# Kernel optimization log

Measured on AMD Instinct MI355X. Metric: run time of the kernel, lower is better.

The kernel has to match this reference:

```python
import jax, jax.numpy as jnp
import numpy as np

B, N, D_FEAT = 16, 4096, 64
NPOINT, NSAMPLE = 1024, 32
MLP = [64, 64, 128]
IN_CH = 3 + D_FEAT
EPS = 1e-5  # BatchNorm eps (torch default)


def _fps(xyz, npoint):
    # Farthest point sampling; sequential scan over npoint steps (matches torch loop).
    b, n, _ = xyz.shape
    def step(carry, _):
        distance, farthest = carry  # (B,N) running min dist, (B,) current centroid idx
        centroid = jnp.take_along_axis(xyz, farthest[:, None, None], axis=1)  # (B,1,3)
        d = jnp.sum((xyz - centroid) ** 2, -1)  # (B,N)
        distance = jnp.minimum(distance, d)
        nxt = jnp.argmax(distance, -1).astype(jnp.int32)
        return (distance, nxt), farthest
    init = (jnp.full((b, n), jnp.inf, dtype=xyz.dtype),
            jnp.full((b,), n // 2, dtype=jnp.int32))
    _, centroids = jax.lax.scan(step, init, None, length=npoint)
    return centroids.T  # (B, npoint)


def _gather(pts, idx):
    # pts: (B,N,C); idx: (B,...) int -> (B,...,C)
    return jax.vmap(lambda p, i: p[i])(pts, idx)


def setup_inputs() -> dict:
    key = jax.random.key(0)
    ks = jax.random.split(key, 16)
    inp = {
        'xyz': jax.random.normal(ks[0], (B, N, 3), jnp.float32),
        'points': jax.random.normal(ks[1], (B, N, D_FEAT), jnp.float32),
    }
    last = IN_CH
    for li, oc in enumerate(MLP):
        inp[f'W{li}'] = jax.random.normal(ks[2 + li], (oc, last), jnp.float32) * (1.0 / np.sqrt(last))
        inp[f'b{li}'] = jnp.zeros((oc,), jnp.float32)
        inp[f'g{li}'] = jnp.ones((oc,), jnp.float32)
        inp[f'be{li}'] = jnp.zeros((oc,), jnp.float32)
        last = oc
    C = MLP[-1]; R = C // 8
    inp['aW1'] = jax.random.normal(ks[10], (R, C), jnp.float32) * (1.0 / np.sqrt(C))
    inp['aW2'] = jax.random.normal(ks[11], (C, R), jnp.float32) * (1.0 / np.sqrt(R))
    return inp


def reference(xyz, points, W0, b0, g0, be0, W1, b1, g1, be1, W2, b2, g2, be2, aW1, aW2):
    fps_idx = _fps(xyz, NPOINT)                 # (B,S) int32
    new_xyz = _gather(xyz, fps_idx)             # (B,S,3)
    # squared distances (B,S,N) via matmul expansion (as torch square_distance)
    d = (-2.0 * jnp.einsum('bsc,bnc->bsn', new_xyz, xyz)
         + jnp.sum(new_xyz ** 2, -1)[..., None]
         + jnp.sum(xyz ** 2, -1)[:, None, :])
    _, idx = jax.lax.top_k(-d, NSAMPLE)         # (B,S,k) nearest neighbors
    grouped_xyz = _gather(xyz, idx)             # (B,S,k,3)
    rel = grouped_xyz - new_xyz[:, :, None, :]  # relative coords
    feat = _gather(points, idx)                 # (B,S,k,D)
    g = jnp.concatenate([rel, feat], axis=-1)   # (B,S,k,3+D) channels-last
    # 1x1 conv MLP + BatchNorm (training-mode batch stats) + ReLU
    for (W, b, ga, be) in ((W0, b0, g0, be0), (W1, b1, g1, be1), (W2, b2, g2, be2)):
        g = jnp.einsum('bskc,oc->bsko', g, W) + b
        mu = g.mean(axis=(0, 1, 2))
        var = g.var(axis=(0, 1, 2))
        g = ga * (g - mu) * jax.lax.rsqrt(var + EPS) + be
        g = jax.nn.relu(g)
    new_points = g.max(axis=2)                  # max over nsample -> (B,S,C)
    # channel attention on (B,C,S) == reductions over S here
    avg = new_points.mean(axis=1)               # (B,C)
    mx = new_points.max(axis=1)                 # (B,C)
    def fc(v):
        return jnp.einsum('cr,br->bc', aW2, jax.nn.relu(jnp.einsum('rc,bc->br', aW1, v)))
    scale = jax.nn.sigmoid(fc(avg) + fc(mx))    # (B,C)
    new_points = new_points * scale[:, None, :]
    return new_xyz, new_points, fps_idx
```

## Files before the change

kernel.cpp:

```cpp
#include <hip/hip_runtime.h>
#include <hip/hip_bf16.h>

#define BB 16
#define NN 4096
#define SS 1024
#define KS 32
#define DF 64
#define INC 67
#define C1 64
#define C2 64
#define C3 128
#define ROWS (BB*SS*KS)
#define EPSBN 1e-5f
#define F_INF (__builtin_inff())

typedef __bf16 bf16;
typedef __bf16 bfrag __attribute__((ext_vector_type(8)));
typedef float  ffrag __attribute__((ext_vector_type(4)));
typedef unsigned long long u64;

#define OUT_NXYZ 0
#define OUT_NP   49152
#define OUT_FPS  2146304

#define OFF_FPS   0u
#define OFF_NXYZ  65536u
#define OFF_IDX   262144u
#define OFF_STATS 2359296u
#define OFF_ASUM  2555904u
#define OFF_AMAX  2621440u
#define OFF_BNC   2686976u
#define OFF_SCALE 2690048u
#define OFF_NP0   2698240u
#define OFF_YMAX  11086848u
#define OFF_H1    19475456u
#define OFF_H2    86584320u
#define ZERO_BYTES (196608u + 65536u + 65536u)

__device__ __forceinline__ u64 dpp_max16(u64 key){
  {
    int lo = __builtin_amdgcn_update_dpp((int)(unsigned)key, (int)(unsigned)key, 0xB1, 0xf, 0xf, true);
    int hi = __builtin_amdgcn_update_dpp((int)(key>>32), (int)(key>>32), 0xB1, 0xf, 0xf, true);
    u64 k2 = ((u64)(unsigned)hi<<32)|(unsigned)lo;
    key = k2 > key ? k2 : key;
  }
  {
    int lo = __builtin_amdgcn_update_dpp((int)(unsigned)key, (int)(unsigned)key, 0x4E, 0xf, 0xf, true);
    int hi = __builtin_amdgcn_update_dpp((int)(key>>32), (int)(key>>32), 0x4E, 0xf, 0xf, true);
    u64 k2 = ((u64)(unsigned)hi<<32)|(unsigned)lo;
    key = k2 > key ? k2 : key;
  }
  {
    int lo = __builtin_amdgcn_update_dpp((int)(unsigned)key, (int)(unsigned)key, 0x141, 0xf, 0xf, true);
    int hi = __builtin_amdgcn_update_dpp((int)(key>>32), (int)(key>>32), 0x141, 0xf, 0xf, true);
    u64 k2 = ((u64)(unsigned)hi<<32)|(unsigned)lo;
    key = k2 > key ? k2 : key;
  }
  {
    int lo = __builtin_amdgcn_update_dpp((int)(unsigned)key, (int)(unsigned)key, 0x140, 0xf, 0xf, true);
    int hi = __builtin_amdgcn_update_dpp((int)(key>>32), (int)(key>>32), 0x140, 0xf, 0xf, true);
    u64 k2 = ((u64)(unsigned)hi<<32)|(unsigned)lo;
    key = k2 > key ? k2 : key;
  }
  return key;
}

__global__ __launch_bounds__(256) void fps_kernel(const float* __restrict__ xyz,
                                                  int* __restrict__ fps_i,
                                                  float* __restrict__ nxyz_ws,
                                                  float* __restrict__ out)
{
  __shared__ float lx[NN], ly[NN], lz[NN];
  __shared__ int lfps[SS];
  __shared__ u64 slotk[2][16];
  int b = blockIdx.x, t = threadIdx.x;
  const float* xb = xyz + (size_t)b*NN*3;
  for (int p = t; p < NN; p += 256){ lx[p]=xb[p*3]; ly[p]=xb[p*3+1]; lz[p]=xb[p*3+2]; }
  __syncthreads();
  float px[16],py[16],pz[16],pd[16];
  int p0 = t*16;
  #pragma unroll
  for (int j=0;j<16;++j){ px[j]=lx[p0+j]; py[j]=ly[p0+j]; pz[j]=lz[p0+j]; pd[j]=F_INF; }
  float cx = lx[NN/2], cy = ly[NN/2], cz = lz[NN/2];
  if (t==0) lfps[0]=NN/2;
  for (int it=1; it<SS; ++it){
    float bv=-1.f; int bi=p0;
    #pragma unroll
    for (int j=0;j<16;++j){
      float dx=px[j]-cx, dy=py[j]-cy, dz=pz[j]-cz;
      float d = __fadd_rn(__fadd_rn(__fmul_rn(dx,dx),__fmul_rn(dy,dy)),__fmul_rn(dz,dz));
      float nd = fminf(pd[j], d);
      pd[j]=nd;
      if (nd > bv){ bv=nd; bi=p0+j; }
    }
    u64 key = ((u64)__float_as_uint(bv) << 32) | (unsigned)(~bi);
    key = dpp_max16(key);
    int p = it & 1;
    if ((t & 15) == 0) slotk[p][t>>4] = key;
    __syncthreads();
    u64 k = slotk[p][t & 15];
    k = dpp_max16(k);
    int i = ~(unsigned)k;
    cx = lx[i]; cy = ly[i]; cz = lz[i];
    if (t==0) lfps[it]=i;
  }
  __syncthreads();
  for (int s=t; s<SS; s+=256){
    int i = lfps[s];
    fps_i[b*SS+s]=i;
    out[OUT_FPS + b*SS + s] = (float)i;
    float xx=lx[i], yy=ly[i], zz=lz[i];
    int o3 = (b*SS+s)*3;
    out[OUT_NXYZ+o3]=xx; out[OUT_NXYZ+o3+1]=yy; out[OUT_NXYZ+o3+2]=zz;
    nxyz_ws[o3]=xx; nxyz_ws[o3+1]=yy; nxyz_ws[o3+2]=zz;
  }
}

__global__ __launch_bounds__(64) void knn_kernel(const float* __restrict__ xyz,
                                                 const float* __restrict__ nxyz,
                                                 int* __restrict__ knn)
{
  __shared__ float ld[NN];
  int lane = threadIdx.x;
  int bs = blockIdx.x;
  int b = bs >> 10;
  const float* xb = xyz + (size_t)b*NN*3;
  float sx=nxyz[bs*3], sy=nxyz[bs*3+1], sz=nxyz[bs*3+2];
  float gv[8]; int gi[8];
  float lv = F_INF; int li = 0;
  #pragma unroll
  for (int g=0; g<8; ++g){
    float bgv = F_INF; int bgi = 0;
    #pragma unroll
    for (int jj=0; jj<8; ++jj){
      int p = (g*8+jj)*64 + lane;
      float dx=xb[p*3]-sx, dy=xb[p*3+1]-sy, dz=xb[p*3+2]-sz;
      float d = dx*dx+dy*dy+dz*dz;
      ld[p] = d;
      if (d < bgv){ bgv=d; bgi=p; }
    }
    gv[g]=bgv; gi[g]=bgi;
    if (bgv < lv){ lv=bgv; li=bgi; }
  }
  int kept = 0;
  for (int it=0; it<KS; ++it){
    float v=lv; int i=li;
    #pragma unroll
    for (int o=32;o;o>>=1){
      float v2=__shfl_xor(v,o); int i2=__shfl_xor(i,o);
      if (v2<v || (v2==v && i2<i)){ v=v2; i=i2; }
    }
    if (lane==it) kept = i;
    if ((i & 63) == lane){
      int j = i >> 6;
      ld[i] = F_INF;
      int g = j >> 3;
      float bgv=F_INF; int bgi=0;
      for (int jj=0;jj<8;++jj){
        int p = (g*8+jj)*64 + lane;
        float d = ld[p];
        if (d<bgv){bgv=d;bgi=p;}
      }
      #pragma unroll
      for (int q=0;q<8;++q){ if (q==g){ gv[q]=bgv; gi[q]=bgi; } }
      lv=F_INF; li=0;
      #pragma unroll
      for (int q=0;q<8;++q){ if (gv[q]<lv){ lv=gv[q]; li=gi[q]; } }
    }
  }
  if (lane < KS) knn[bs*KS + lane] = kept;
}

__global__ __launch_bounds__(256) void conv1_kernel(const float* __restrict__ xyz,
                                                    const float* __restrict__ points,
                                                    const float* __restrict__ W0,
                                                    const float* __restrict__ b0,
                                                    const float* __restrict__ nxyz,
                                                    const int* __restrict__ knn,
                                                    bf16* __restrict__ h1,
                                                    float* __restrict__ stats)
{
  __shared__ __align__(16) bf16 As[64][104];
  __shared__ __align__(16) bf16 Bs[64][104];
  __shared__ float s1[C1], s2[C1];
  int t = threadIdx.x;
  int Rbase = blockIdx.x * 64;
  if (t < C1){ s1[t]=0.f; s2[t]=0.f; }
  {
    int o = t >> 2, q = t & 3;
    const float* wr = W0 + o*INC;
    for (int cc = q*24; cc < q*24+24; ++cc){
      float w;
      if (cc < 64) w = wr[3+cc];
      else if (cc < 67) w = wr[cc-64];
      else w = 0.f;
      Bs[o][cc] = (bf16)w;
    }
  }
  {
    int r = t >> 2, q = t & 3;
    int R = Rbase + r;
    int bs = R >> 5;
    int bIdx = bs >> 10;
    int nI = knn[R];
    const float* pr = points + ((size_t)(bIdx*NN + nI))*DF + q*16;
    float4 f0 = *(const float4*)(pr);
    float4 f1 = *(const float4*)(pr+4);
    float4 f2 = *(const float4*)(pr+8);
    float4 f3 = *(const float4*)(pr+12);
    bf16* ap = &As[r][q*16];
    ap[0]=(bf16)f0.x; ap[1]=(bf16)f0.y; ap[2]=(bf16)f0.z; ap[3]=(bf16)f0.w;
    ap[4]=(bf16)f1.x; ap[5]=(bf16)f1.y; ap[6]=(bf16)f1.z; ap[7]=(bf16)f1.w;
    ap[8]=(bf16)f2.x; ap[9]=(bf16)f2.y; ap[10]=(bf16)f2.z; ap[11]=(bf16)f2.w;
    ap[12]=(bf16)f3.x; ap[13]=(bf16)f3.y; ap[14]=(bf16)f3.z; ap[15]=(bf16)f3.w;
    if (q==0){
      const float* xr = xyz + ((size_t)(bIdx*NN + nI))*3;
      const float* nr = nxyz + bs*3;
      As[r][64]=(bf16)(xr[0]-nr[0]);
      As[r][65]=(bf16)(xr[1]-nr[1]);
      As[r][66]=(bf16)(xr[2]-nr[2]);
      for (int cc=67; cc<96; ++cc) As[r][cc]=(bf16)0.f;
    }
  }
  __syncthreads();
  int wv = t >> 6, lane = t & 63;
  int row16 = wv * 16;
  int arow = lane & 15, kgrp = lane >> 4;
  ffrag acc[4] = {};
  #pragma unroll
  for (int kc = 0; kc < 3; ++kc){
    bfrag af = *(const bfrag*)&As[row16 + arow][kc*32 + kgrp*8];
    #pragma unroll
    for (int nt = 0; nt < 4; ++nt){
      bfrag bfv = *(const bfrag*)&Bs[nt*16 + arow][kc*32 + kgrp*8];
      acc[nt] = __builtin_amdgcn_mfma_f32_16x16x32_bf16(af, bfv, acc[nt], 0,0,0);
    }
  }
  #pragma unroll
  for (int nt=0; nt<4; ++nt){
    int c = nt*16 + arow;
    float bias = b0[c];
    float ls1=0.f, ls2=0.f;
    #pragma unroll
    for (int r=0;r<4;++r){
      float y = acc[nt][r] + bias;
      int grow = Rbase + row16 + kgrp*4 + r;
      h1[(size_t)grow*C1 + c] = (bf16)y;
      ls1 += y; ls2 += y*y;
    }
    ls1 += __shfl_xor(ls1, 16); ls1 += __shfl_xor(ls1, 32);
    ls2 += __shfl_xor(ls2, 16); ls2 += __shfl_xor(ls2, 32);
    if (kgrp==0){ atomicAdd(&s1[c], ls1); atomicAdd(&s2[c], ls2); }
  }
  __syncthreads();
  if (t < C1){
    float* gp = stats + (blockIdx.x & 63)*256;
    atomicAdd(&gp[t], s1[t]);
    atomicAdd(&gp[128 + t], s2[t]);
  }
}

__global__ void bnfin_kernel(const float* __restrict__ stats, const float* __restrict__ g,
                             const float* __restrict__ be, float* __restrict__ bnc, int C)
{
  int c = threadIdx.x; if (c >= C) return;
  float a1=0.f, a2=0.f;
  for (int q=0;q<64;++q){ a1 += stats[q*256+c]; a2 += stats[q*256+128+c]; }
  float inv = 1.f/(float)ROWS;
  float mu = a1*inv; float var = a2*inv - mu*mu;
  float a = g[c]*rsqrtf(var + EPSBN);
  bnc[c] = a; bnc[128+c] = be[c] - mu*a;
}

__global__ __launch_bounds__(256) void conv2_kernel(const bf16* __restrict__ h1,
                                                    const float* __restrict__ W1,
                                                    const float* __restrict__ b1,
                                                    const float* __restrict__ bnc,
                                                    bf16* __restrict__ h2,
                                                    float* __restrict__ stats)
{
  __shared__ __align__(16) bf16 As[64][72];
  __shared__ __align__(16) bf16 Bs[64][72];
  __shared__ float s1[C2], s2[C2];
  int t = threadIdx.x;
  int Rbase = blockIdx.x * 64;
  if (t < C2){ s1[t]=0.f; s2[t]=0.f; }
  {
    int o = t >> 2, q = t & 3;
    const float* wr = W1 + o*64 + q*16;
    bf16* bp = &Bs[o][q*16];
    #pragma unroll
    for (int v=0; v<4; ++v){
      float4 f = *(const float4*)(wr + v*4);
      bp[v*4+0]=(bf16)f.x; bp[v*4+1]=(bf16)f.y; bp[v*4+2]=(bf16)f.z; bp[v*4+3]=(bf16)f.w;
    }
  }
  {
    int r = t >> 2, q = t & 3;
    int R = Rbase + r;
    const bf16* hr = h1 + (size_t)R*64 + q*16;
    bfrag h0 = *(const bfrag*)hr;
    bfrag h1v = *(const bfrag*)(hr+8);
    #pragma unroll
    for (int j=0;j<8;++j){
      int c=q*16+j;
      As[r][c] = (bf16)fmaxf(fmaf(bnc[c], (float)h0[j], bnc[128+c]), 0.f);
    }
    #pragma unroll
    for (int j=0;j<8;++j){
      int c=q*16+8+j;
      As[r][c] = (bf16)fmaxf(fmaf(bnc[c], (float)h1v[j], bnc[128+c]), 0.f);
    }
  }
  __syncthreads();
  int wv = t >> 6, lane = t & 63;
  int row16 = wv * 16;
  int arow = lane & 15, kgrp = lane >> 4;
  ffrag acc[4] = {};
  #pragma unroll
  for (int kc = 0; kc < 2; ++kc){
    bfrag af = *(const bfrag*)&As[row16 + arow][kc*32 + kgrp*8];
    #pragma unroll
    for (int nt = 0; nt < 4; ++nt){
      bfrag bfv = *(const bfrag*)&Bs[nt*16 + arow][kc*32 + kgrp*8];
      acc[nt] = __builtin_amdgcn_mfma_f32_16x16x32_bf16(af, bfv, acc[nt], 0,0,0);
    }
  }
  #pragma unroll
  for (int nt=0; nt<4; ++nt){
    int c = nt*16 + arow;
    float bias = b1[c];
    float ls1=0.f, ls2=0.f;
    #pragma unroll
    for (int r=0;r<4;++r){
      float y = acc[nt][r] + bias;
      int grow = Rbase + row16 + kgrp*4 + r;
      h2[(size_t)grow*C2 + c] = (bf16)y;
      ls1 += y; ls2 += y*y;
    }
    ls1 += __shfl_xor(ls1, 16); ls1 += __shfl_xor(ls1, 32);
    ls2 += __shfl_xor(ls2, 16); ls2 += __shfl_xor(ls2, 32);
    if (kgrp==0){ atomicAdd(&s1[c], ls1); atomicAdd(&s2[c], ls2); }
  }
  __syncthreads();
  if (t < C2){
    float* gp = stats + (blockIdx.x & 63)*256;
    atomicAdd(&gp[t], s1[t]);
    atomicAdd(&gp[128 + t], s2[t]);
  }
}

__global__ __launch_bounds__(256) void conv3_kernel(const bf16* __restrict__ h2,
                                                    const float* __restrict__ W2,
                                                    const float* __restrict__ b2,
                                                    const float* __restrict__ bnc,
                                                    float* __restrict__ ymax,
                                                    float* __restrict__ stats)
{
  __shared__ __align__(16) bf16 As[64][72];
  __shared__ __align__(16) bf16 Bs[128][72];
  __shared__ float s1[C3], s2[C3];
  __shared__ float wmax[4][C3];
  int t = threadIdx.x;
  int Rbase = blockIdx.x * 64;
  if (t < C3){ s1[t]=0.f; s2[t]=0.f; }
  {
    int o = t >> 1, q = t & 1;
    const float* wr = W2 + o*64 + q*32;
    bf16* bp = &Bs[o][q*32];
    #pragma unroll
    for (int v=0; v<8; ++v){
      float4 f = *(const float4*)(wr + v*4);
      bp[v*4+0]=(bf16)f.x; bp[v*4+1]=(bf16)f.y; bp[v*4+2]=(bf16)f.z; bp[v*4+3]=(bf16)f.w;
    }
  }
  {
    int r = t >> 2, q = t & 3;
    int R = Rbase + r;
    const bf16* hr = h2 + (size_t)R*64 + q*16;
    bfrag h0 = *(const bfrag*)hr;
    bfrag h1v = *(const bfrag*)(hr+8);
    #pragma unroll
    for (int j=0;j<8;++j){
      int c=q*16+j;
      As[r][c] = (bf16)fmaxf(fmaf(bnc[c], (float)h0[j], bnc[128+c]), 0.f);
    }
    #pragma unroll
    for (int j=0;j<8;++j){
      int c=q*16+8+j;
      As[r][c] = (bf16)fmaxf(fmaf(bnc[c], (float)h1v[j], bnc[128+c]), 0.f);
    }
  }
  __syncthreads();
  int wv = t >> 6, lane = t & 63;
  int row16 = wv * 16;
  int arow = lane & 15, kgrp = lane >> 4;
  ffrag acc[8] = {};
  #pragma unroll
  for (int kc = 0; kc < 2; ++kc){
    bfrag af = *(const bfrag*)&As[row16 + arow][kc*32 + kgrp*8];
    #pragma unroll
    for (int nt = 0; nt < 8; ++nt){
      bfrag bfv = *(const bfrag*)&Bs[nt*16 + arow][kc*32 + kgrp*8];
      acc[nt] = __builtin_amdgcn_mfma_f32_16x16x32_bf16(af, bfv, acc[nt], 0,0,0);
    }
  }
  #pragma unroll
  for (int nt=0; nt<8; ++nt){
    int c = nt*16 + arow;
    float bias = b2[c];
    float ls1=0.f, ls2=0.f, mm=-F_INF;
    #pragma unroll
    for (int r=0;r<4;++r){
      float y = acc[nt][r] + bias;
      ls1 += y; ls2 += y*y; mm = fmaxf(mm, y);
    }
    ls1 += __shfl_xor(ls1, 16); ls1 += __shfl_xor(ls1, 32);
    ls2 += __shfl_xor(ls2, 16); ls2 += __shfl_xor(ls2, 32);
    mm = fmaxf(mm, __shfl_xor(mm, 16)); mm = fmaxf(mm, __shfl_xor(mm, 32));
    if (kgrp==0){ atomicAdd(&s1[c], ls1); atomicAdd(&s2[c], ls2); wmax[wv][c]=mm; }
  }
  __syncthreads();
  {
    int half = t >> 7;
    int c = t & 127;
    float m = fmaxf(wmax[half*2][c], wmax[half*2+1][c]);
    ymax[(size_t)(blockIdx.x*2 + half)*C3 + c] = m;
  }
  if (t < C3){
    float* gp = stats + (blockIdx.x & 63)*256;
    atomicAdd(&gp[t], s1[t]);
    atomicAdd(&gp[128 + t], s2[t]);
  }
}

__global__ __launch_bounds__(256) void attreduce_kernel(const float* __restrict__ ymax,
                                                        const float* __restrict__ bnc,
                                                        float* __restrict__ np0,
                                                        float* __restrict__ asum,
                                                        unsigned* __restrict__ amax)
{
  __shared__ float rs[256], rm[256];
  int t = threadIdx.x;
  int b = blockIdx.x >> 3, sg = blockIdx.x & 7;
  int c = t & 127, h = t >> 7;
  float a = bnc[c], bb = bnc[128+c];
  size_t base = ((size_t)(b*1024 + sg*128 + h*64))*128 + c;
  float s = 0.f, m = 0.f;
  #pragma unroll 4
  for (int j=0;j<64;++j){
    float v = fmaxf(fmaf(a, ymax[base + (size_t)j*128], bb), 0.f);
    np0[base + (size_t)j*128] = v;
    s += v; m = fmaxf(m, v);
  }
  rs[t]=s; rm[t]=m;
  __syncthreads();
  if (t < 128){
    float s2 = rs[t] + rs[t+128];
    float m2 = fmaxf(rm[t], rm[t+128]);
    atomicAdd(&asum[b*128+t], s2);
    atomicMax(&amax[b*128+t], __float_as_uint(m2));
  }
}

__global__ __launch_bounds__(256) void attn_kernel(const float* __restrict__ asum,
                                                   const unsigned* __restrict__ amax,
                                                   const float* __restrict__ aW1,
                                                   const float* __restrict__ aW2,
                                                   float* __restrict__ scale)
{
  __shared__ float avg[16][128], mx[16][128], hA[16][16], hM[16][16];
  int t = threadIdx.x;
  for (int i=t; i<2048; i+=256){
    int b=i>>7, c=i&127;
    avg[b][c]=asum[i]*(1.f/1024.f); mx[b][c]=__uint_as_float(amax[i]);
  }
  __syncthreads();
  {
    int b=t>>4, r=t&15;
    float sa=0.f, sm=0.f;
    for (int c=0;c<128;++c){ float w=aW1[r*128+c]; sa+=w*avg[b][c]; sm+=w*mx[b][c]; }
    hA[b][r]=fmaxf(sa,0.f); hM[b][r]=fmaxf(sm,0.f);
  }
  __syncthreads();
  for (int i=t;i<2048;i+=256){
    int b=i>>7,c=i&127;
    float o=0.f;
    for (int r=0;r<16;++r){ o += aW2[c*16+r]*(hA[b][r]+hM[b][r]); }
    scale[i] = 1.f/(1.f+expf(-o));
  }
}

__global__ __launch_bounds__(256) void finout_kernel(const float* __restrict__ np0,
                                                     const float* __restrict__ scale,
                                                     float* __restrict__ out)
{
  int i = blockIdx.x*256 + threadIdx.x;
  int c = i & 127; int b = i >> 17;
  out[OUT_NP + i] = np0[i] * scale[b*128+c];
}

extern "C" void kernel_launch(void* const* d_in, const int* in_sizes, int n_in,
                              void* d_out, int out_size, void* d_ws, size_t ws_size,
                              hipStream_t stream)
{
  const float* xyz    = (const float*)d_in[0];
  const float* points = (const float*)d_in[1];
  const float* W0 = (const float*)d_in[2];
  const float* b0 = (const float*)d_in[3];
  const float* g0 = (const float*)d_in[4];
  const float* be0= (const float*)d_in[5];
  const float* W1 = (const float*)d_in[6];
  const float* b1 = (const float*)d_in[7];
  const float* g1 = (const float*)d_in[8];
  const float* be1= (const float*)d_in[9];
  const float* W2 = (const float*)d_in[10];
  const float* b2 = (const float*)d_in[11];
  const float* g2 = (const float*)d_in[12];
  const float* be2= (const float*)d_in[13];
  const float* aW1= (const float*)d_in[14];
  const float* aW2= (const float*)d_in[15];
  float* out = (float*)d_out;
  char* ws = (char*)d_ws;

  int*      fpsI  = (int*)(ws + OFF_FPS);
  float*    nxyz  = (float*)(ws + OFF_NXYZ);
  int*      knnI  = (int*)(ws + OFF_IDX);
  float*    stats = (float*)(ws + OFF_STATS);
  float*    asum  = (float*)(ws + OFF_ASUM);
  unsigned* amax  = (unsigned*)(ws + OFF_AMAX);
  float*    bnc   = (float*)(ws + OFF_BNC);
  float*    scl   = (float*)(ws + OFF_SCALE);
  float*    np0   = (float*)(ws + OFF_NP0);
  float*    ymax  = (float*)(ws + OFF_YMAX);
  bf16*     h1    = (bf16*)(ws + OFF_H1);
  bf16*     h2    = (bf16*)(ws + OFF_H2);

  hipMemsetAsync(ws + OFF_STATS, 0, ZERO_BYTES, stream);
  fps_kernel<<<BB, 256, 0, stream>>>(xyz, fpsI, nxyz, out);
  knn_kernel<<<BB*SS, 64, 0, stream>>>(xyz, nxyz, knnI);
  conv1_kernel<<<ROWS/64, 256, 0, stream>>>(xyz, points, W0, b0, nxyz, knnI, h1, stats);
  bnfin_kernel<<<1, 128, 0, stream>>>(stats, g0, be0, bnc, C1);
  conv2_kernel<<<ROWS/64, 256, 0, stream>>>(h1, W1, b1, bnc, h2, stats + 64*256);
  bnfin_kernel<<<1, 128, 0, stream>>>(stats + 64*256, g1, be1, bnc + 256, C2);
  conv3_kernel<<<ROWS/64, 256, 0, stream>>>(h2, W2, b2, bnc + 256, ymax, stats + 2*64*256);
  bnfin_kernel<<<1, 128, 0, stream>>>(stats + 2*64*256, g2, be2, bnc + 512, C3);
  attreduce_kernel<<<BB*8, 256, 0, stream>>>(ymax, bnc + 512, np0, asum, amax);
  attn_kernel<<<1, 256, 0, stream>>>(asum, amax, aW1, aW2, scl);
  finout_kernel<<<(BB*SS*C3)/256, 256, 0, stream>>>(np0, scl, out);
}
```

Baseline: 1.202 ms.

## Use full-wave DPP reductions and packed float2 math in FPS and kNN

Replaces the 16-lane DPP argmax with a full 64-lane DPP reduction (row_shr plus row_bcast) followed by a lane-63 broadcast. This cuts the cross-wave slot exchange in FPS from 16 to 4 entries and replaces the shuffle-based argmin in the kNN selection loop. Point coordinates are stored as float4 in LDS so the centroid lookup is a single load, and distance math uses float2 vectors to allow packed FP32 instructions. FP contraction is disabled so the distance rounding stays the same; the risk is that the bcast DPP semantics or the lane-63 broadcast pick the wrong winner.

```diff
diff --git a/kernel.cpp b/kernel.cpp
--- a/kernel.cpp
+++ b/kernel.cpp
@@ -17,6 +17,7 @@
 typedef __bf16 bf16;
 typedef __bf16 bfrag __attribute__((ext_vector_type(8)));
 typedef float  ffrag __attribute__((ext_vector_type(4)));
+typedef float  f2    __attribute__((ext_vector_type(2)));
 typedef unsigned long long u64;
 
 #define OUT_NXYZ 0
@@ -37,32 +38,20 @@
 #define OFF_H2    86584320u
 #define ZERO_BYTES (196608u + 65536u + 65536u)
 
-__device__ __forceinline__ u64 dpp_max16(u64 key){
-  {
-    int lo = __builtin_amdgcn_update_dpp((int)(unsigned)key, (int)(unsigned)key, 0xB1, 0xf, 0xf, true);
-    int hi = __builtin_amdgcn_update_dpp((int)(key>>32), (int)(key>>32), 0xB1, 0xf, 0xf, true);
-    u64 k2 = ((u64)(unsigned)hi<<32)|(unsigned)lo;
-    key = k2 > key ? k2 : key;
-  }
-  {
-    int lo = __builtin_amdgcn_update_dpp((int)(unsigned)key, (int)(unsigned)key, 0x4E, 0xf, 0xf, true);
-    int hi = __builtin_amdgcn_update_dpp((int)(key>>32), (int)(key>>32), 0x4E, 0xf, 0xf, true);
-    u64 k2 = ((u64)(unsigned)hi<<32)|(unsigned)lo;
-    key = k2 > key ? k2 : key;
-  }
-  {
-    int lo = __builtin_amdgcn_update_dpp((int)(unsigned)key, (int)(unsigned)key, 0x141, 0xf, 0xf, true);
-    int hi = __builtin_amdgcn_update_dpp((int)(key>>32), (int)(key>>32), 0x141, 0xf, 0xf, true);
-    u64 k2 = ((u64)(unsigned)hi<<32)|(unsigned)lo;
-    key = k2 > key ? k2 : key;
-  }
-  {
-    int lo = __builtin_amdgcn_update_dpp((int)(unsigned)key, (int)(unsigned)key, 0x140, 0xf, 0xf, true);
-    int hi = __builtin_amdgcn_update_dpp((int)(key>>32), (int)(key>>32), 0x140, 0xf, 0xf, true);
-    u64 k2 = ((u64)(unsigned)hi<<32)|(unsigned)lo;
-    key = k2 > key ? k2 : key;
-  }
-  return key;
+#define DPP_MAX_STEP(k, ctrl, rmask, bc) { \
+  int _lo = __builtin_amdgcn_update_dpp(0, (int)(unsigned)(k), (ctrl), (rmask), 0xf, (bc)); \
+  int _hi = __builtin_amdgcn_update_dpp(0, (int)((k)>>32),     (ctrl), (rmask), 0xf, (bc)); \
+  u64 _k2 = ((u64)(unsigned)_hi << 32) | (unsigned)_lo; \
+  if (_k2 > (k)) (k) = _k2; }
+
+__device__ __forceinline__ u64 dpp_wavemax64(u64 k){
+  DPP_MAX_STEP(k, 0x111, 0xf, true)
+  DPP_MAX_STEP(k, 0x112, 0xf, true)
+  DPP_MAX_STEP(k, 0x114, 0xf, true)
+  DPP_MAX_STEP(k, 0x118, 0xf, true)
+  DPP_MAX_STEP(k, 0x142, 0xa, false)
+  DPP_MAX_STEP(k, 0x143, 0xc, false)
+  return k;
 }
 
 __global__ __launch_bounds__(256) void fps_kernel(const float* __restrict__ xyz,
@@ -70,38 +59,51 @@
                                                   float* __restrict__ nxyz_ws,
                                                   float* __restrict__ out)
 {
-  __shared__ float lx[NN], ly[NN], lz[NN];
+  #pragma clang fp contract(off)
+  __shared__ __align__(16) float4 lc[NN];
   __shared__ int lfps[SS];
-  __shared__ u64 slotk[2][16];
+  __shared__ u64 slotk[2][4];
   int b = blockIdx.x, t = threadIdx.x;
   const float* xb = xyz + (size_t)b*NN*3;
-  for (int p = t; p < NN; p += 256){ lx[p]=xb[p*3]; ly[p]=xb[p*3+1]; lz[p]=xb[p*3+2]; }
-  __syncthreads();
-  float px[16],py[16],pz[16],pd[16];
+  for (int p = t; p < NN; p += 256){
+    lc[p] = make_float4(xb[p*3], xb[p*3+1], xb[p*3+2], 0.f);
+  }
+  __syncthreads();
+  f2 px2[8], py2[8], pz2[8], pd2[8];
   int p0 = t*16;
   #pragma unroll
-  for (int j=0;j<16;++j){ px[j]=lx[p0+j]; py[j]=ly[p0+j]; pz[j]=lz[p0+j]; pd[j]=F_INF; }
-  float cx = lx[NN/2], cy = ly[NN/2], cz = lz[NN/2];
+  for (int j=0;j<8;++j){
+    float4 a = lc[p0+2*j], c = lc[p0+2*j+1];
+    px2[j] = (f2){a.x, c.x}; py2[j] = (f2){a.y, c.y}; pz2[j] = (f2){a.z, c.z};
+    pd2[j] = (f2){F_INF, F_INF};
+  }
+  float cx = lc[NN/2].x, cy = lc[NN/2].y, cz = lc[NN/2].z;
   if (t==0) lfps[0]=NN/2;
+  int wv = t >> 6, lane = t & 63;
   for (int it=1; it<SS; ++it){
+    f2 c2x = (f2){cx,cx}, c2y = (f2){cy,cy}, c2z = (f2){cz,cz};
     float bv=-1.f; int bi=p0;
     #pragma unroll
-    for (int j=0;j<16;++j){
-      float dx=px[j]-cx, dy=py[j]-cy, dz=pz[j]-cz;
-      float d = __fadd_rn(__fadd_rn(__fmul_rn(dx,dx),__fmul_rn(dy,dy)),__fmul_rn(dz,dz));
-      float nd = fminf(pd[j], d);
-      pd[j]=nd;
-      if (nd > bv){ bv=nd; bi=p0+j; }
+    for (int j=0;j<8;++j){
+      f2 dx = px2[j]-c2x, dy = py2[j]-c2y, dz = pz2[j]-c2z;
+      f2 d = (dx*dx + dy*dy) + dz*dz;
+      f2 nd = (f2){fminf(pd2[j].x, d.x), fminf(pd2[j].y, d.y)};
+      pd2[j]=nd;
+      if (nd.x > bv){ bv=nd.x; bi=p0+2*j; }
+      if (nd.y > bv){ bv=nd.y; bi=p0+2*j+1; }
     }
     u64 key = ((u64)__float_as_uint(bv) << 32) | (unsigned)(~bi);
-    key = dpp_max16(key);
+    key = dpp_wavemax64(key);
+    key = __shfl(key, 63);
     int p = it & 1;
-    if ((t & 15) == 0) slotk[p][t>>4] = key;
+    if (lane == 0) slotk[p][wv] = key;
     __syncthreads();
-    u64 k = slotk[p][t & 15];
-    k = dpp_max16(k);
+    u64 k = slotk[p][t & 3];
+    DPP_MAX_STEP(k, 0xB1, 0xf, true)
+    DPP_MAX_STEP(k, 0x4E, 0xf, true)
     int i = ~(unsigned)k;
-    cx = lx[i]; cy = ly[i]; cz = lz[i];
+    float4 cc = lc[i];
+    cx = cc.x; cy = cc.y; cz = cc.z;
     if (t==0) lfps[it]=i;
   }
   __syncthreads();
@@ -109,10 +111,10 @@
     int i = lfps[s];
     fps_i[b*SS+s]=i;
     out[OUT_FPS + b*SS + s] = (float)i;
-    float xx=lx[i], yy=ly[i], zz=lz[i];
+    float4 cc = lc[i];
     int o3 = (b*SS+s)*3;
-    out[OUT_NXYZ+o3]=xx; out[OUT_NXYZ+o3+1]=yy; out[OUT_NXYZ+o3+2]=zz;
-    nxyz_ws[o3]=xx; nxyz_ws[o3+1]=yy; nxyz_ws[o3+2]=zz;
+    out[OUT_NXYZ+o3]=cc.x; out[OUT_NXYZ+o3+1]=cc.y; out[OUT_NXYZ+o3+2]=cc.z;
+    nxyz_ws[o3]=cc.x; nxyz_ws[o3+1]=cc.y; nxyz_ws[o3+2]=cc.z;
   }
 }
 
@@ -144,12 +146,10 @@
   }
   int kept = 0;
   for (int it=0; it<KS; ++it){
-    float v=lv; int i=li;
-    #pragma unroll
-    for (int o=32;o;o>>=1){
-      float v2=__shfl_xor(v,o); int i2=__shfl_xor(i,o);
-      if (v2<v || (v2==v && i2<i)){ v=v2; i=i2; }
-    }
+    u64 mk = ~(((u64)__float_as_uint(lv) << 32) | (unsigned)li);
+    mk = dpp_wavemax64(mk);
+    mk = __shfl(mk, 63);
+    int i = (int)(unsigned)(~mk);
     if (lane==it) kept = i;
     if ((i & 63) == lane){
       int j = i >> 6;
@@ -206,12 +206,12 @@
     const float* pr = points + ((size_t)(bIdx*NN + nI))*DF + q*16;
     float4 f0 = *(const float4*)(pr);
     float4 f1 = *(const float4*)(pr+4);
-    float4 f2 = *(const float4*)(pr+8);
+    float4 f2v = *(const float4*)(pr+8);
     float4 f3 = *(const float4*)(pr+12);
     bf16* ap = &As[r][q*16];
     ap[0]=(bf16)f0.x; ap[1]=(bf16)f0.y; ap[2]=(bf16)f0.z; ap[3]=(bf16)f0.w;
     ap[4]=(bf16)f1.x; ap[5]=(bf16)f1.y; ap[6]=(bf16)f1.z; ap[7]=(bf16)f1.w;
-    ap[8]=(bf16)f2.x; ap[9]=(bf16)f2.y; ap[10]=(bf16)f2.z; ap[11]=(bf16)f2.w;
+    ap[8]=(bf16)f2v.x; ap[9]=(bf16)f2v.y; ap[10]=(bf16)f2v.z; ap[11]=(bf16)f2v.w;
     ap[12]=(bf16)f3.x; ap[13]=(bf16)f3.y; ap[14]=(bf16)f3.z; ap[15]=(bf16)f3.w;
     if (q==0){
       const float* xr = xyz + ((size_t)(bIdx*NN + nI))*3;
```

Result: faster. 1.087 ms (-9.6%).
